# Kernel tuning notes

Measured on AMD Instinct MI355X. Metric: run time of the kernel, lower is better.

## Reference

```python
import jax, jax.numpy as jnp
import numpy as np

NX = 1024
N_HEAD = 16
HEAD_DIM = NX // N_HEAD
MASKED_BIAS = -10000.0


def setup_inputs() -> dict:
    key = jax.random.key(0)
    k1, k2, k3 = jax.random.split(key, 3)
    hidden_states = jax.random.normal(k1, (2, 2048, NX), dtype=jnp.float32)
    # Conv1D weights: stored [in, out], y = x @ W + b (like torch addmm)
    c_attn_w = jax.random.normal(k2, (NX, 3 * NX), dtype=jnp.float32) * 0.02
    c_attn_b = jnp.zeros((3 * NX,), dtype=jnp.float32)
    c_proj_w = jax.random.normal(k3, (NX, NX), dtype=jnp.float32) * 0.02
    c_proj_b = jnp.zeros((NX,), dtype=jnp.float32)
    return {
        "hidden_states": hidden_states,
        "c_attn_w": c_attn_w,
        "c_attn_b": c_attn_b,
        "c_proj_w": c_proj_w,
        "c_proj_b": c_proj_b,
    }


def reference(hidden_states, c_attn_w, c_attn_b, c_proj_w, c_proj_b):
    B, S, _ = hidden_states.shape
    qkv = hidden_states @ c_attn_w + c_attn_b  # [B, S, 3*NX]
    q, k, v = jnp.split(qkv, 3, axis=-1)
    # split heads -> [B, H, S, D]
    def split_heads(x):
        return x.reshape(B, S, N_HEAD, HEAD_DIM).transpose(0, 2, 1, 3)
    q, k, v = split_heads(q), split_heads(k), split_heads(v)
    # scores scaled by sqrt(head_dim) (v.size(-1)**0.5 in original)
    w = jnp.einsum("bhqd,bhkd->bhqk", q, k) / jnp.sqrt(jnp.float32(HEAD_DIM))
    # causal mask (nd == ns here since no past)
    causal = jnp.tril(jnp.ones((S, S), dtype=bool))
    w = jnp.where(causal[None, None, :, :], w, jnp.float32(MASKED_BIAS))
    w = jax.nn.softmax(w, axis=-1)
    a = jnp.einsum("bhqk,bhkd->bhqd", w, v)  # [B, H, S, D]
    # merge heads
    a = a.transpose(0, 2, 1, 3).reshape(B, S, NX)
    out = a @ c_proj_w + c_proj_b
    return out
```

## Files before the change

kernel.cpp:

```cpp
#include <hip/hip_runtime.h>
#include <hip/hip_bf16.h>
#include <cmath>

typedef __attribute__((ext_vector_type(8))) short bf16x8;
typedef __attribute__((ext_vector_type(4))) float f32x4;

#define NXC 1024
#define NH 16
#define HD 64
#define BATCH 2
#define SEQ 2048
#define TOK (BATCH * SEQ)

__device__ __forceinline__ ushort f2bf(float f) {
  unsigned u;
  asm("v_cvt_pk_bf16_f32 %0, %1, %2" : "=v"(u) : "v"(f), "v"(f));
  return (ushort)u;
}

__device__ __forceinline__ void gload_lds16(const void* g, void* lds) {
  __builtin_amdgcn_global_load_lds(
      (const __attribute__((address_space(1))) void*)g,
      (__attribute__((address_space(3))) void*)lds, 16, 0, 0);
}

__device__ __forceinline__ float fast_exp2(float x) {
  float r;
  asm("v_exp_f32 %0, %1" : "=v"(r) : "v"(x));
  return r;
}

template <int CTRL>
__device__ __forceinline__ float dpp_mov(float x) {
  return __builtin_bit_cast(
      float, __builtin_amdgcn_mov_dpp(__builtin_bit_cast(int, x), CTRL, 0xF, 0xF, true));
}
__device__ __forceinline__ float red16_max(float x) {
  x = fmaxf(x, dpp_mov<0x121>(x));
  x = fmaxf(x, dpp_mov<0x122>(x));
  x = fmaxf(x, dpp_mov<0x124>(x));
  x = fmaxf(x, dpp_mov<0x128>(x));
  return x;
}
__device__ __forceinline__ float red16_sum(float x) {
  x += dpp_mov<0x121>(x);
  x += dpp_mov<0x122>(x);
  x += dpp_mov<0x124>(x);
  x += dpp_mov<0x128>(x);
  return x;
}

__global__ __launch_bounds__(256) void k_transpose_w(const float* __restrict__ in,
                                                     ushort* __restrict__ out,
                                                     int Kd, int Nd) {
  __shared__ float t[32][33];
  int n0 = blockIdx.x * 32, k0 = blockIdx.y * 32;
  int tx = threadIdx.x & 31, ty = threadIdx.x >> 5;
#pragma unroll
  for (int r = 0; r < 4; ++r)
    t[tx][ty + r * 8] = in[(size_t)(k0 + ty + r * 8) * Nd + n0 + tx];
  __syncthreads();
  int nl = threadIdx.x >> 3, kq = (threadIdx.x & 7) * 4;
  ushort4 o;
  o.x = f2bf(t[nl][kq + 0]);
  o.y = f2bf(t[nl][kq + 1]);
  o.z = f2bf(t[nl][kq + 2]);
  o.w = f2bf(t[nl][kq + 3]);
  int row = n0 + nl, kk = k0 + kq;
  size_t dst = (size_t)row * Kd + (kk & ~63) + ((kk & 63) ^ ((row & 7) << 3));
  *(ushort4*)&out[dst] = o;
}

__global__ __launch_bounds__(256, 3) void k_gemm_qkv(const float* __restrict__ X,
                                                     const ushort* __restrict__ Bt,
                                                     const float* __restrict__ bias,
                                                     ushort* __restrict__ q_ws,
                                                     ushort* __restrict__ k_ws,
                                                     ushort* __restrict__ v_ws) {
  __shared__ ushort As[128 * 64];
  __shared__ ushort Bs[2][128 * 64];
  const int tid = threadIdx.x;
  const int wave = tid >> 6, lane = tid & 63;
  const int xcd = blockIdx.x & 7, loc = blockIdx.x >> 3;
  const int m0 = ((xcd >> 1) * 8 + (loc & 7)) * 128;
  const int n0 = ((xcd & 1) * 12 + (loc >> 3)) * 128;
  const int wr = (wave >> 1) * 64, wc = (wave & 1) * 64;
  const int l15 = lane & 15, lg = lane >> 4;
  const int swz = (l15 & 7) << 3;
  const int arow = wave * 32 + lg;
  const int akcol = l15 * 4;
  f32x4 acc[4][4] = {};
  float4 areg[8];

  auto a_issue = [&](int kt) {
#pragma unroll
    for (int c = 0; c < 8; ++c)
      areg[c] = *(const float4*)&X[(size_t)(m0 + arow + c * 4) * 1024 + kt * 64 + akcol];
  };
  auto a_write = [&]() {
#pragma unroll
    for (int c = 0; c < 8; ++c) {
      int row = arow + c * 4;
      unsigned p0, p1;
      asm("v_cvt_pk_bf16_f32 %0, %1, %2" : "=v"(p0) : "v"(areg[c].x), "v"(areg[c].y));
      asm("v_cvt_pk_bf16_f32 %0, %1, %2" : "=v"(p1) : "v"(areg[c].z), "v"(areg[c].w));
      *(uint2*)&As[row * 64 + (akcol ^ ((row & 7) << 3))] = make_uint2(p0, p1);
    }
  };
  auto stageB = [&](int kt, int buf) {
#pragma unroll
    for (int c = 0; c < 4; ++c) {
      int offB = wave * 4096 + c * 1024 + lane * 16;
      int row = offB >> 7, colB = offB & 127;
      gload_lds16((const char*)Bt + (size_t)(n0 + row) * 2048 + kt * 128 + colB,
                  (char*)Bs[buf] + wave * 4096 + c * 1024);
    }
  };

  a_issue(0);
  stageB(0, 0);
  a_write();
  a_issue(1);
  asm volatile("s_waitcnt vmcnt(8) lgkmcnt(0)" ::: "memory");
  __builtin_amdgcn_s_barrier();

#pragma unroll 1
  for (int kt = 0; kt < 16; ++kt) {
    const int cur = kt & 1;
    if (kt < 15) stageB(kt + 1, cur ^ 1);
#pragma unroll
    for (int kc = 0; kc < 2; ++kc) {
      bf16x8 af[4], bfr[4];
#pragma unroll
      for (int i = 0; i < 4; ++i)
        af[i] = *(const bf16x8*)&As[(wr + i * 16 + l15) * 64 + ((kc * 32 + lg * 8) ^ swz)];
#pragma unroll
      for (int j = 0; j < 4; ++j)
        bfr[j] = *(const bf16x8*)&Bs[cur][(wc + j * 16 + l15) * 64 + ((kc * 32 + lg * 8) ^ swz)];
#pragma unroll
      for (int i = 0; i < 4; ++i)
#pragma unroll
        for (int j = 0; j < 4; ++j)
          acc[i][j] = __builtin_amdgcn_mfma_f32_16x16x32_bf16(af[i], bfr[j], acc[i][j], 0, 0, 0);
    }
    __syncthreads();
    if (kt < 15) {
      a_write();
      if (kt < 14) a_issue(kt + 2);
      asm volatile("s_waitcnt lgkmcnt(0)" ::: "memory");
      __builtin_amdgcn_s_barrier();
    }
  }

#pragma unroll
  for (int j = 0; j < 4; ++j) {
    int col = n0 + wc + j * 16 + l15;
    float bv = bias[col];
    int sec = col >> 10;
    int within = col & 1023;
    int head = within >> 6, d = within & 63;
#pragma unroll
    for (int i = 0; i < 4; ++i) {
#pragma unroll
      for (int r = 0; r < 4; ++r) {
        int row = m0 + wr + i * 16 + lg * 4 + r;
        int b = row >> 11, s = row & 2047;
        float val = acc[i][j][r] + bv;
        int bh = b * NH + head;
        if (sec == 0) {
          q_ws[((size_t)bh * SEQ + s) * HD + d] = f2bf(val * 0.1803368801f);
        } else if (sec == 1) {
          k_ws[((size_t)bh * SEQ + s) * HD + (d ^ ((s & 7) << 3))] = f2bf(val);
        } else {
          int slot = (((s & 15) * 4 + ((s >> 4) & 3)) ^ ((d & 7) << 3));
          v_ws[((size_t)bh * HD + d) * SEQ + (s & ~63) + slot] = f2bf(val);
        }
      }
    }
  }
}

__global__ __launch_bounds__(256) void k_attn(const ushort* __restrict__ q_ws,
                                              const ushort* __restrict__ k_ws,
                                              const ushort* __restrict__ v_ws,
                                              ushort* __restrict__ a_ws) {
  __shared__ ushort Ks[2][64 * 64];
  __shared__ ushort Vs[2][64 * 64];
  __shared__ ushort Ps[4][2][16 * 64];
  const int p = blockIdx.x, bh = blockIdx.y;
  const int qtA = 31 - p, qtB = p;
  const int tid = threadIdx.x, wave = tid >> 6, lane = tid & 63;
  const int l15 = lane & 15, lg = lane >> 4;
  const int swz = (l15 & 7) << 3;
  const ushort* qp = q_ws + (size_t)bh * SEQ * HD;
  const ushort* kp = k_ws + (size_t)bh * SEQ * HD;
  const ushort* vp = v_ws + (size_t)bh * HD * SEQ;

  bf16x8 qfA[2], qfB[2];
  {
    int qrA = qtA * 64 + wave * 16 + l15;
    int qrB = qtB * 64 + wave * 16 + l15;
    qfA[0] = *(const bf16x8*)&qp[(size_t)qrA * HD + lg * 8];
    qfA[1] = *(const bf16x8*)&qp[(size_t)qrA * HD + 32 + lg * 8];
    qfB[0] = *(const bf16x8*)&qp[(size_t)qrB * HD + lg * 8];
    qfB[1] = *(const bf16x8*)&qp[(size_t)qrB * HD + 32 + lg * 8];
  }
  f32x4 oA[4] = {}, oB[4] = {};
  float mA[4] = {-INFINITY, -INFINITY, -INFINITY, -INFINITY};
  float mB[4] = {-INFINITY, -INFINITY, -INFINITY, -INFINITY};
  float lA[4] = {0.f, 0.f, 0.f, 0.f}, lB[4] = {0.f, 0.f, 0.f, 0.f};
  bf16x8 kf[2][4], vf[2][4];

  auto stage = [&](int kt, int buf) {
#pragma unroll
    for (int c = 0; c < 2; ++c) {
      int offB = wave * 2048 + c * 1024 + lane * 16;
      gload_lds16((const char*)kp + (size_t)kt * 8192 + offB,
                  (char*)Ks[buf] + offB);
      int d = offB >> 7, keyB = offB & 127;
      gload_lds16((const char*)vp + (size_t)d * (SEQ * 2) + (size_t)kt * 128 + keyB,
                  (char*)Vs[buf] + offB);
    }
  };

  auto tile_step = [&](const bf16x8* qf, f32x4* o, float* m_r, float* l_r,
                       ushort* Pw, bool diag) {
    f32x4 sc[4] = {};
    __builtin_amdgcn_s_setprio(1);
#pragma unroll
    for (int kc = 0; kc < 2; ++kc)
#pragma unroll
      for (int f = 0; f < 4; ++f) {
        if (diag && f > wave) continue;
        sc[f] = __builtin_amdgcn_mfma_f32_16x16x32_bf16(qf[kc], kf[kc][f], sc[f], 0, 0, 0);
      }
    __builtin_amdgcn_s_setprio(0);
    if (diag) {
#pragma unroll
      for (int f = 0; f < 4; ++f) {
        int key_rel = f * 16 + l15;
#pragma unroll
        for (int r = 0; r < 4; ++r) {
          int q_rel = wave * 16 + lg * 4 + r;
          if (key_rel > q_rel) sc[f][r] = -1e30f;
        }
      }
    }
    float pm[4];
#pragma unroll
    for (int r = 0; r < 4; ++r)
      pm[r] = fmaxf(fmaxf(sc[0][r], sc[1][r]), fmaxf(sc[2][r], sc[3][r]));
    bool need = false;
#pragma unroll
    for (int r = 0; r < 4; ++r) need |= (pm[r] > m_r[r] + 8.f);
    if (__any(need)) {
#pragma unroll
      for (int r = 0; r < 4; ++r) {
        float full = red16_max(pm[r]);
        float mn = fmaxf(m_r[r], full);
        float al = fast_exp2(m_r[r] - mn);
        m_r[r] = mn;
        l_r[r] *= al;
#pragma unroll
        for (int df = 0; df < 4; ++df) o[df][r] *= al;
      }
    }
#pragma unroll
    for (int r = 0; r < 4; ++r) {
      int q = lg * 4 + r;
      float e0 = fast_exp2(sc[0][r] - m_r[r]);
      float e1 = fast_exp2(sc[1][r] - m_r[r]);
      float e2 = fast_exp2(sc[2][r] - m_r[r]);
      float e3 = fast_exp2(sc[3][r] - m_r[r]);
      l_r[r] += (e0 + e1) + (e2 + e3);
      unsigned p0, p1;
      asm("v_cvt_pk_bf16_f32 %0, %1, %2" : "=v"(p0) : "v"(e0), "v"(e1));
      asm("v_cvt_pk_bf16_f32 %0, %1, %2" : "=v"(p1) : "v"(e2), "v"(e3));
      *(uint2*)&Pw[q * 64 + ((l15 * 4) ^ ((q & 7) << 3))] = make_uint2(p0, p1);
    }
    __builtin_amdgcn_s_setprio(1);
#pragma unroll
    for (int kc = 0; kc < 2; ++kc) {
      bf16x8 pf = *(const bf16x8*)&Pw[l15 * 64 + ((kc * 32 + lg * 8) ^ swz)];
#pragma unroll
      for (int df = 0; df < 4; ++df)
        o[df] = __builtin_amdgcn_mfma_f32_16x16x32_bf16(pf, vf[kc][df], o[df], 0, 0, 0);
    }
    __builtin_amdgcn_s_setprio(0);
  };

  stage(0, 0);
  asm volatile("s_waitcnt vmcnt(0)" ::: "memory");
  __syncthreads();

  for (int kt = 0; kt <= qtA; ++kt) {
    const int cur = kt & 1;
    if (kt < qtA) stage(kt + 1, cur ^ 1);
#pragma unroll
    for (int kc = 0; kc < 2; ++kc)
#pragma unroll
      for (int f = 0; f < 4; ++f) {
        kf[kc][f] = *(const bf16x8*)&Ks[cur][(f * 16 + l15) * 64 + ((kc * 32 + lg * 8) ^ swz)];
        vf[kc][f] = *(const bf16x8*)&Vs[cur][(f * 16 + l15) * 64 + ((kc * 32 + lg * 8) ^ swz)];
      }
    tile_step(qfA, oA, mA, lA, Ps[wave][0], kt == qtA);
    if (kt <= qtB)
      tile_step(qfB, oB, mB, lB, Ps[wave][1], kt == qtB);
    asm volatile("s_waitcnt vmcnt(0)" ::: "memory");
    __builtin_amdgcn_s_barrier();
  }

  int b = bh >> 4, head = bh & 15;
  auto epilogue = [&](f32x4* o, float* l_r, int qt) {
#pragma unroll
    for (int r = 0; r < 4; ++r) {
      float inv = 1.0f / red16_sum(l_r[r]);
      int s = qt * 64 + wave * 16 + lg * 4 + r;
#pragma unroll
      for (int df = 0; df < 4; ++df) {
        int col = head * 64 + ((df * 16 + l15) ^ ((s & 7) << 3));
        a_ws[((size_t)(b * SEQ + s)) * NXC + col] = f2bf(o[df][r] * inv);
      }
    }
  };
  epilogue(oA, lA, qtA);
  epilogue(oB, lB, qtB);
}

__global__ __launch_bounds__(256) void k_gemm_proj(const ushort* __restrict__ A,
                                                   const ushort* __restrict__ Bt,
                                                   const float* __restrict__ bias,
                                                   float* __restrict__ out) {
  __shared__ ushort As[2][128 * 64];
  __shared__ ushort Bs[2][128 * 64];
  const int tid = threadIdx.x;
  const int wave = tid >> 6, lane = tid & 63;
  const int xcd = blockIdx.x & 7, loc = blockIdx.x >> 3;
  const int m0 = ((xcd >> 1) * 8 + (loc & 7)) * 128;
  const int n0 = ((xcd & 1) * 4 + (loc >> 3)) * 128;
  const int wr = (wave >> 1) * 64, wc = (wave & 1) * 64;
  const int l15 = lane & 15, lg = lane >> 4;
  const int swz = (l15 & 7) << 3;
  f32x4 acc[4][4] = {};

  auto stage = [&](int k0, int buf) {
#pragma unroll
    for (int c = 0; c < 4; ++c) {
      int offB = wave * 4096 + c * 1024 + lane * 16;
      int row = offB >> 7, colB = offB & 127;
      gload_lds16((const char*)A + (size_t)(m0 + row) * 2048 + k0 * 2 + colB,
                  (char*)As[buf] + wave * 4096 + c * 1024);
      gload_lds16((const char*)Bt + (size_t)(n0 + row) * 2048 + k0 * 2 + colB,
                  (char*)Bs[buf] + wave * 4096 + c * 1024);
    }
  };

  stage(0, 0);
  asm volatile("s_waitcnt vmcnt(0)" ::: "memory");
  __syncthreads();

  for (int kt = 0; kt < 16; ++kt) {
    const int cur = kt & 1;
    if (kt < 15) stage((kt + 1) * 64, cur ^ 1);
#pragma unroll
    for (int kc = 0; kc < 2; ++kc) {
      bf16x8 af[4], bfr[4];
#pragma unroll
      for (int i = 0; i < 4; ++i)
        af[i] = *(const bf16x8*)&As[cur][(wr + i * 16 + l15) * 64 + ((kc * 32 + lg * 8) ^ swz)];
#pragma unroll
      for (int j = 0; j < 4; ++j)
        bfr[j] = *(const bf16x8*)&Bs[cur][(wc + j * 16 + l15) * 64 + ((kc * 32 + lg * 8) ^ swz)];
#pragma unroll
      for (int i = 0; i < 4; ++i)
#pragma unroll
        for (int j = 0; j < 4; ++j)
          acc[i][j] = __builtin_amdgcn_mfma_f32_16x16x32_bf16(af[i], bfr[j], acc[i][j], 0, 0, 0);
    }
    asm volatile("s_waitcnt vmcnt(0)" ::: "memory");
    __syncthreads();
  }
#pragma unroll
  for (int j = 0; j < 4; ++j) {
    int col = n0 + wc + j * 16 + l15;
    float bv = bias[col];
#pragma unroll
    for (int i = 0; i < 4; ++i) {
#pragma unroll
      for (int r = 0; r < 4; ++r) {
        int row = m0 + wr + i * 16 + lg * 4 + r;
        out[(size_t)row * NXC + col] = acc[i][j][r] + bv;
      }
    }
  }
}

extern "C" void kernel_launch(void* const* d_in, const int* in_sizes, int n_in,
                              void* d_out, int out_size, void* d_ws, size_t ws_size,
                              hipStream_t stream) {
  const float* hs       = (const float*)d_in[0];
  const float* c_attn_w = (const float*)d_in[1];
  const float* c_attn_b = (const float*)d_in[2];
  const float* c_proj_w = (const float*)d_in[3];
  const float* c_proj_b = (const float*)d_in[4];
  char* ws = (char*)d_ws;
  const size_t MB = 1 << 20;
  ushort* Wt_attn = (ushort*)(ws + 8 * MB);
  ushort* Wt_proj = (ushort*)(ws + 14 * MB);
  ushort* q_ws    = (ushort*)(ws + 16 * MB);
  ushort* k_ws    = (ushort*)(ws + 24 * MB);
  ushort* v_ws    = (ushort*)(ws + 32 * MB);
  ushort* a_ws    = (ushort*)(ws + 40 * MB);

  k_transpose_w<<<dim3(96, 32), 256, 0, stream>>>(c_attn_w, Wt_attn, 1024, 3072);
  k_transpose_w<<<dim3(32, 32), 256, 0, stream>>>(c_proj_w, Wt_proj, 1024, 1024);
  k_gemm_qkv<<<768, 256, 0, stream>>>(hs, Wt_attn, c_attn_b, q_ws, k_ws, v_ws);
  k_attn<<<dim3(16, 32), 256, 0, stream>>>(q_ws, k_ws, v_ws, a_ws);
  k_gemm_proj<<<256, 256, 0, stream>>>(a_ws, Wt_proj, c_proj_b, (float*)d_out);
}
```

Before: 130.9 us.

## Triple-buffer LDS tiles with prefetch depth two in all three kernels

Converts the double-buffered LDS staging in the QKV GEMM, attention, and projection GEMM kernels to triple buffering, issuing global-to-LDS loads two tiles ahead. Partial vmcnt waits replace full drains, so one tile's loads stay in flight across the barrier. This is meant to hide global memory latency behind the MFMA work. In exchange it uses more LDS per block, and the QKV kernel's launch bound drops from 3 to 2 blocks per CU, which may reduce occupancy.

```diff
diff --git a/kernel.cpp b/kernel.cpp
--- a/kernel.cpp
+++ b/kernel.cpp
@@ -71,14 +71,14 @@
   *(ushort4*)&out[dst] = o;
 }
 
-__global__ __launch_bounds__(256, 3) void k_gemm_qkv(const float* __restrict__ X,
+__global__ __launch_bounds__(256, 2) void k_gemm_qkv(const float* __restrict__ X,
                                                      const ushort* __restrict__ Bt,
                                                      const float* __restrict__ bias,
                                                      ushort* __restrict__ q_ws,
                                                      ushort* __restrict__ k_ws,
                                                      ushort* __restrict__ v_ws) {
   __shared__ ushort As[128 * 64];
-  __shared__ ushort Bs[2][128 * 64];
+  __shared__ ushort Bs[3][128 * 64];
   const int tid = threadIdx.x;
   const int wave = tid >> 6, lane = tid & 63;
   const int xcd = blockIdx.x & 7, loc = blockIdx.x >> 3;
@@ -111,23 +111,23 @@
 #pragma unroll
     for (int c = 0; c < 4; ++c) {
       int offB = wave * 4096 + c * 1024 + lane * 16;
-      int row = offB >> 7, colB = offB & 127;
-      gload_lds16((const char*)Bt + (size_t)(n0 + row) * 2048 + kt * 128 + colB,
+      gload_lds16((const char*)Bt + (size_t)((n0 + (offB >> 7)) * 2048) + kt * 128 + (offB & 127),
                   (char*)Bs[buf] + wave * 4096 + c * 1024);
     }
   };
 
   a_issue(0);
   stageB(0, 0);
+  stageB(1, 1);
   a_write();
   a_issue(1);
-  asm volatile("s_waitcnt vmcnt(8) lgkmcnt(0)" ::: "memory");
+  asm volatile("s_waitcnt vmcnt(12) lgkmcnt(0)" ::: "memory");
   __builtin_amdgcn_s_barrier();
 
 #pragma unroll 1
   for (int kt = 0; kt < 16; ++kt) {
-    const int cur = kt & 1;
-    if (kt < 15) stageB(kt + 1, cur ^ 1);
+    if (kt < 14) stageB(kt + 2, (kt + 2) % 3);
+    const ushort* Bcur = Bs[kt % 3];
 #pragma unroll
     for (int kc = 0; kc < 2; ++kc) {
       bf16x8 af[4], bfr[4];
@@ -136,18 +136,19 @@
         af[i] = *(const bf16x8*)&As[(wr + i * 16 + l15) * 64 + ((kc * 32 + lg * 8) ^ swz)];
 #pragma unroll
       for (int j = 0; j < 4; ++j)
-        bfr[j] = *(const bf16x8*)&Bs[cur][(wc + j * 16 + l15) * 64 + ((kc * 32 + lg * 8) ^ swz)];
+        bfr[j] = *(const bf16x8*)&Bcur[(wc + j * 16 + l15) * 64 + ((kc * 32 + lg * 8) ^ swz)];
 #pragma unroll
       for (int i = 0; i < 4; ++i)
 #pragma unroll
         for (int j = 0; j < 4; ++j)
           acc[i][j] = __builtin_amdgcn_mfma_f32_16x16x32_bf16(af[i], bfr[j], acc[i][j], 0, 0, 0);
     }
-    __syncthreads();
+    __builtin_amdgcn_s_barrier();
     if (kt < 15) {
       a_write();
       if (kt < 14) a_issue(kt + 2);
-      asm volatile("s_waitcnt lgkmcnt(0)" ::: "memory");
+      if (kt < 14) asm volatile("s_waitcnt vmcnt(12) lgkmcnt(0)" ::: "memory");
+      else         asm volatile("s_waitcnt vmcnt(0) lgkmcnt(0)" ::: "memory");
       __builtin_amdgcn_s_barrier();
     }
   }
@@ -184,8 +185,8 @@
                                               const ushort* __restrict__ k_ws,
                                               const ushort* __restrict__ v_ws,
                                               ushort* __restrict__ a_ws) {
-  __shared__ ushort Ks[2][64 * 64];
-  __shared__ ushort Vs[2][64 * 64];
+  __shared__ ushort Ks[3][64 * 64];
+  __shared__ ushort Vs[3][64 * 64];
   __shared__ ushort Ps[4][2][16 * 64];
   const int p = blockIdx.x, bh = blockIdx.y;
   const int qtA = 31 - p, qtB = p;
@@ -290,12 +291,13 @@
   };
 
   stage(0, 0);
-  asm volatile("s_waitcnt vmcnt(0)" ::: "memory");
-  __syncthreads();
+  stage(1, 1);
+  asm volatile("s_waitcnt vmcnt(4)" ::: "memory");
+  __builtin_amdgcn_s_barrier();
 
   for (int kt = 0; kt <= qtA; ++kt) {
-    const int cur = kt & 1;
-    if (kt < qtA) stage(kt + 1, cur ^ 1);
+    if (kt + 2 <= qtA) stage(kt + 2, (kt + 2) % 3);
+    const int cur = kt % 3;
 #pragma unroll
     for (int kc = 0; kc < 2; ++kc)
 #pragma unroll
@@ -306,8 +308,11 @@
     tile_step(qfA, oA, mA, lA, Ps[wave][0], kt == qtA);
     if (kt <= qtB)
       tile_step(qfB, oB, mB, lB, Ps[wave][1], kt == qtB);
-    asm volatile("s_waitcnt vmcnt(0)" ::: "memory");
-    __builtin_amdgcn_s_barrier();
+    if (kt < qtA) {
+      if (kt + 2 <= qtA) asm volatile("s_waitcnt vmcnt(4)" ::: "memory");
+      else               asm volatile("s_waitcnt vmcnt(0)" ::: "memory");
+      __builtin_amdgcn_s_barrier();
+    }
   }
 
   int b = bh >> 4, head = bh & 15;
@@ -331,8 +336,8 @@
                                                    const ushort* __restrict__ Bt,
                                                    const float* __restrict__ bias,
                                                    float* __restrict__ out) {
-  __shared__ ushort As[2][128 * 64];
-  __shared__ ushort Bs[2][128 * 64];
+  __shared__ ushort As[3][128 * 64];
+  __shared__ ushort Bs[3][128 * 64];
   const int tid = threadIdx.x;
   const int wave = tid >> 6, lane = tid & 63;
   const int xcd = blockIdx.x & 7, loc = blockIdx.x >> 3;
@@ -343,25 +348,27 @@
   const int swz = (l15 & 7) << 3;
   f32x4 acc[4][4] = {};
 
-  auto stage = [&](int k0, int buf) {
+  auto stage = [&](int kt, int buf) {
 #pragma unroll
     for (int c = 0; c < 4; ++c) {
       int offB = wave * 4096 + c * 1024 + lane * 16;
       int row = offB >> 7, colB = offB & 127;
-      gload_lds16((const char*)A + (size_t)(m0 + row) * 2048 + k0 * 2 + colB,
+      gload_lds16((const char*)A + (size_t)(m0 + row) * 2048 + kt * 128 + colB,
                   (char*)As[buf] + wave * 4096 + c * 1024);
-      gload_lds16((const char*)Bt + (size_t)(n0 + row) * 2048 + k0 * 2 + colB,
+      gload_lds16((const char*)Bt + (size_t)(n0 + row) * 2048 + kt * 128 + colB,
                   (char*)Bs[buf] + wave * 4096 + c * 1024);
     }
   };
 
   stage(0, 0);
-  asm volatile("s_waitcnt vmcnt(0)" ::: "memory");
-  __syncthreads();
-
+  stage(1, 1);
+  asm volatile("s_waitcnt vmcnt(8)" ::: "memory");
+  __builtin_amdgcn_s_barrier();
+
+#pragma unroll 1
   for (int kt = 0; kt < 16; ++kt) {
-    const int cur = kt & 1;
-    if (kt < 15) stage((kt + 1) * 64, cur ^ 1);
+    if (kt < 14) stage(kt + 2, (kt + 2) % 3);
+    const int cur = kt % 3;
 #pragma unroll
     for (int kc = 0; kc < 2; ++kc) {
       bf16x8 af[4], bfr[4];
@@ -377,8 +384,11 @@
         for (int j = 0; j < 4; ++j)
           acc[i][j] = __builtin_amdgcn_mfma_f32_16x16x32_bf16(af[i], bfr[j], acc[i][j], 0, 0, 0);
     }
-    asm volatile("s_waitcnt vmcnt(0)" ::: "memory");
-    __syncthreads();
+    if (kt < 15) {
+      if (kt < 14) asm volatile("s_waitcnt vmcnt(8)" ::: "memory");
+      else         asm volatile("s_waitcnt vmcnt(0)" ::: "memory");
+      __builtin_amdgcn_s_barrier();
+    }
   }
 #pragma unroll
   for (int j = 0; j < 4; ++j) {
```

After: 147.9 us. +12.9%, slower.

## Write V head-major from QKV GEMM, add separate V transpose kernel, remap attn blocks per XCD

Applied to the files above, without the earlier changes.

The QKV GEMM epilogue no longer scatters V directly into the transposed, swizzled layout. It writes V in the same row-major per-head layout as Q and K into a temporary buffer that reuses the attention-output workspace. A new small kernel then transposes V through shared memory into the swizzled layout the attention kernel expects, so scattered strided stores are traded for an extra kernel launch and one more pass over V. The attention grid is also flattened and remapped so that all blocks of a given batch-head land on the same XCD, which should improve L2 reuse of K and V.

```diff
diff --git a/kernel.cpp b/kernel.cpp
--- a/kernel.cpp
+++ b/kernel.cpp
@@ -71,12 +71,36 @@
   *(ushort4*)&out[dst] = o;
 }
 
+__global__ __launch_bounds__(256) void k_transpose_v(const ushort* __restrict__ in,
+                                                     ushort* __restrict__ out) {
+  __shared__ ushort t[64][33];
+  int bh = blockIdx.z;
+  int s0 = blockIdx.x * 64, d0 = blockIdx.y * 32;
+  const ushort* ip = in + (size_t)bh * SEQ * HD;
+  ushort* op = out + (size_t)bh * HD * SEQ;
+  int dl_in = threadIdx.x & 31, sl_in = threadIdx.x >> 5;
+#pragma unroll
+  for (int m = 0; m < 8; ++m)
+    t[sl_in + m * 8][dl_in] = ip[(size_t)(s0 + sl_in + m * 8) * HD + d0 + dl_in];
+  __syncthreads();
+  int dl = threadIdx.x >> 3;
+  int kp = threadIdx.x & 7;
+#pragma unroll
+  for (int kk = 0; kk < 2; ++kk) {
+    int k = kp * 2 + kk;
+    ushort4 o;
+    o.x = t[k][dl]; o.y = t[k + 16][dl]; o.z = t[k + 32][dl]; o.w = t[k + 48][dl];
+    int slot = (4 * k) ^ ((dl & 7) << 3);
+    *(ushort4*)&op[(size_t)(d0 + dl) * SEQ + s0 + slot] = o;
+  }
+}
+
 __global__ __launch_bounds__(256, 3) void k_gemm_qkv(const float* __restrict__ X,
                                                      const ushort* __restrict__ Bt,
                                                      const float* __restrict__ bias,
                                                      ushort* __restrict__ q_ws,
                                                      ushort* __restrict__ k_ws,
-                                                     ushort* __restrict__ v_ws) {
+                                                     ushort* __restrict__ v_tmp) {
   __shared__ ushort As[128 * 64];
   __shared__ ushort Bs[2][128 * 64];
   const int tid = threadIdx.x;
@@ -166,15 +190,10 @@
         int row = m0 + wr + i * 16 + lg * 4 + r;
         int b = row >> 11, s = row & 2047;
         float val = acc[i][j][r] + bv;
-        int bh = b * NH + head;
-        if (sec == 0) {
-          q_ws[((size_t)bh * SEQ + s) * HD + d] = f2bf(val * 0.1803368801f);
-        } else if (sec == 1) {
-          k_ws[((size_t)bh * SEQ + s) * HD + (d ^ ((s & 7) << 3))] = f2bf(val);
-        } else {
-          int slot = (((s & 15) * 4 + ((s >> 4) & 3)) ^ ((d & 7) << 3));
-          v_ws[((size_t)bh * HD + d) * SEQ + (s & ~63) + slot] = f2bf(val);
-        }
+        size_t hb = ((size_t)(b * NH + head) * SEQ + s) * HD;
+        if (sec == 0)      q_ws[hb + d] = f2bf(val * 0.1803368801f);
+        else if (sec == 1) k_ws[hb + (d ^ ((s & 7) << 3))] = f2bf(val);
+        else               v_tmp[hb + d] = f2bf(val);
       }
     }
   }
@@ -187,7 +206,10 @@
   __shared__ ushort Ks[2][64 * 64];
   __shared__ ushort Vs[2][64 * 64];
   __shared__ ushort Ps[4][2][16 * 64];
-  const int p = blockIdx.x, bh = blockIdx.y;
+  const int bid = blockIdx.x;
+  const int xcd = bid & 7, idx = bid >> 3;
+  const int bh = xcd * 4 + (idx >> 4);
+  const int p = idx & 15;
   const int qtA = 31 - p, qtB = p;
   const int tid = threadIdx.x, wave = tid >> 6, lane = tid & 63;
   const int l15 = lane & 15, lg = lane >> 4;
@@ -411,10 +433,12 @@
   ushort* k_ws    = (ushort*)(ws + 24 * MB);
   ushort* v_ws    = (ushort*)(ws + 32 * MB);
   ushort* a_ws    = (ushort*)(ws + 40 * MB);
+  ushort* v_tmp   = a_ws;
 
   k_transpose_w<<<dim3(96, 32), 256, 0, stream>>>(c_attn_w, Wt_attn, 1024, 3072);
   k_transpose_w<<<dim3(32, 32), 256, 0, stream>>>(c_proj_w, Wt_proj, 1024, 1024);
-  k_gemm_qkv<<<768, 256, 0, stream>>>(hs, Wt_attn, c_attn_b, q_ws, k_ws, v_ws);
-  k_attn<<<dim3(16, 32), 256, 0, stream>>>(q_ws, k_ws, v_ws, a_ws);
+  k_gemm_qkv<<<768, 256, 0, stream>>>(hs, Wt_attn, c_attn_b, q_ws, k_ws, v_tmp);
+  k_transpose_v<<<dim3(32, 2, 32), 256, 0, stream>>>(v_tmp, v_ws);
+  k_attn<<<512, 256, 0, stream>>>(q_ws, k_ws, v_ws, a_ws);
   k_gemm_proj<<<256, 256, 0, stream>>>(a_ws, Wt_proj, c_proj_b, (float*)d_out);
 }
```

After: 123.3 us. 1.06x faster.
